# Optimization experiments

Measured on AMD Instinct MI355X. Metric: run time of the kernel, lower is better.

## Reference

```python
import jax, jax.numpy as jnp
import numpy as np

B, S, N, D, H = 4, 1024, 1024, 1024, 16
HD = D // H
EPS = 1e-5


def _xavier(key, shape):
    fan_in, fan_out = shape[1], shape[0]
    a = (6.0 / (fan_in + fan_out)) ** 0.5
    return jax.random.uniform(key, shape, jnp.float32, -a, a)


def layer_norm(x, g, b):
    m = jnp.mean(x, axis=-1, keepdims=True)
    v = jnp.mean(jnp.square(x - m), axis=-1, keepdims=True)
    return (x - m) * jax.lax.rsqrt(v + EPS) * g + b


def setup_inputs() -> dict:
    key = jax.random.key(0)
    ks = jax.random.split(key, 8)
    return {
        "x_q": jax.random.normal(ks[0], (B, S, D), jnp.float32),
        "x_k": jax.random.normal(ks[1], (B, N, D), jnp.float32),
        "x_v": jax.random.normal(ks[2], (B, N, D), jnp.float32),
        "Wq": _xavier(ks[3], (D, D)),
        "Wk": _xavier(ks[4], (D, D)),
        "Wv": _xavier(ks[5], (D, D)),
        "Wp": _xavier(ks[6], (D, D)),
        "qn_g": jnp.ones((HD,), jnp.float32),
        "qn_b": jnp.zeros((HD,), jnp.float32),
        "kn_g": jnp.ones((HD,), jnp.float32),
        "kn_b": jnp.zeros((HD,), jnp.float32),
        "on_g": jnp.ones((D,), jnp.float32),
        "on_b": jnp.zeros((D,), jnp.float32),
    }


def reference(x_q, x_k, x_v, Wq, Wk, Wv, Wp, qn_g, qn_b, kn_g, kn_b, on_g, on_b):
    scale = HD ** (-0.5)
    q = jnp.einsum('bsd,ed->bse', x_q, Wq)  # torch Linear: x @ W.T
    k = jnp.einsum('bnd,ed->bne', x_k, Wk)
    v = jnp.einsum('bnd,ed->bne', x_v, Wv)
    # Faithful to original: q is reshaped WITHOUT transpose (B,H,S,HD)
    q = q.reshape(B, H, S, HD)
    k = k.reshape(B, N, H, HD).transpose(0, 2, 1, 3)  # (B,H,N,HD)
    v = v.reshape(B, N, H, HD).transpose(0, 2, 1, 3)  # (B,H,N,HD)
    q = layer_norm(q, qn_g, qn_b) * scale
    k = layer_norm(k, kn_g, kn_b)
    attn = jax.nn.softmax(jnp.einsum('bhsd,bhnd->bhsn', q, k), axis=-1)
    x = jnp.einsum('bhsn,bhnd->bhsd', attn, v)
    x = x.transpose(0, 2, 1, 3).reshape(B, S, D)
    x = layer_norm(x, on_g, on_b)
    return jnp.einsum('bsd,ed->bse', x, Wp)
```

## Files before the change

### kernel.cpp

```cpp
#include <hip/hip_runtime.h>
#include <cstdint>

typedef unsigned short u16;
typedef __attribute__((ext_vector_type(4))) float f32x4;
typedef __attribute__((ext_vector_type(8))) short bf16x8;

__device__ __forceinline__ u16 f2bf(float f) {
  uint32_t u = __builtin_bit_cast(uint32_t, f);
  u += 0x7FFFu + ((u >> 16) & 1u);
  return (u16)(u >> 16);
}

__device__ __forceinline__ void gld16(const void* g, void* l) {
  __builtin_amdgcn_global_load_lds((const __attribute__((address_space(1))) void*)g,
                                   (__attribute__((address_space(3))) void*)l,
                                   16, 0, 0);
}

__global__ __launch_bounds__(256) void cast_all(const float* __restrict__ xq, const float* __restrict__ xk,
                                                const float* __restrict__ xv, const float* __restrict__ Wq,
                                                const float* __restrict__ Wk, const float* __restrict__ Wv,
                                                const float* __restrict__ Wp,
                                                u16* __restrict__ oq, u16* __restrict__ ok, u16* __restrict__ ov,
                                                u16* __restrict__ owq, u16* __restrict__ owk,
                                                u16* __restrict__ owv, u16* __restrict__ owp) {
  int bid = blockIdx.x;
  const float* src; u16* dst; size_t i;
  if (bid < 12288) {
    const int p = bid >> 12, ib = bid & 4095;
    src = (p == 0) ? xq : ((p == 1) ? xk : xv);
    dst = (p == 0) ? oq : ((p == 1) ? ok : ov);
    i = (size_t)ib * 256 + threadIdx.x;
  } else {
    bid -= 12288;
    const int p = bid >> 10, ib = bid & 1023;
    src = (p == 0) ? Wq : ((p == 1) ? Wk : ((p == 2) ? Wv : Wp));
    dst = (p == 0) ? owq : ((p == 1) ? owk : ((p == 2) ? owv : owp));
    i = (size_t)ib * 256 + threadIdx.x;
  }
  float4 v = *(const float4*)(src + i * 4);
  uint2 pk;
  pk.x = (uint32_t)f2bf(v.x) | ((uint32_t)f2bf(v.y) << 16);
  pk.y = (uint32_t)f2bf(v.z) | ((uint32_t)f2bf(v.w) << 16);
  *(uint2*)(dst + i * 4) = pk;
}

__device__ __forceinline__ void gemm_mainloop(const u16* __restrict__ A, const u16* __restrict__ B,
                                              int bm, int bn, u16* Al, u16* Bl,
                                              f32x4 (&acc)[2][4]) {
  const int t = threadIdx.x;
  const int w = t >> 6;
  const int lane = t & 63;
  const int l15 = lane & 15, l4 = lane >> 4;

  const u16* Ab = A + (size_t)bm * 128 * 1024;
  const u16* Bb = B + (size_t)bn * 64 * 1024;

  for (int kt = 0; kt < 1024; kt += 64) {
#pragma unroll
    for (int p = 0; p < 4; ++p) {
      const int idx = p * 256 + t;
      const int row = idx >> 3, ch = idx & 7;
      const int sch = ch ^ (row & 7);
      gld16(Ab + (size_t)row * 1024 + kt + sch * 8, (char*)Al + p * 4096 + (w << 10));
    }
#pragma unroll
    for (int p = 0; p < 2; ++p) {
      const int idx = p * 256 + t;
      const int row = idx >> 3, ch = idx & 7;
      const int sch = ch ^ (row & 7);
      gld16(Bb + (size_t)row * 1024 + kt + sch * 8, (char*)Bl + p * 4096 + (w << 10));
    }
    __syncthreads();
#pragma unroll
    for (int ks = 0; ks < 2; ++ks) {
      bf16x8 af[2], bfr[4];
#pragma unroll
      for (int mi = 0; mi < 2; ++mi) {
        const int row = w * 32 + mi * 16 + l15;
        const int ch = (ks * 4 + l4) ^ (row & 7);
        af[mi] = *(const bf16x8*)&Al[row * 64 + ch * 8];
      }
#pragma unroll
      for (int nj = 0; nj < 4; ++nj) {
        const int row = nj * 16 + l15;
        const int ch = (ks * 4 + l4) ^ (row & 7);
        bfr[nj] = *(const bf16x8*)&Bl[row * 64 + ch * 8];
      }
#pragma unroll
      for (int mi = 0; mi < 2; ++mi)
#pragma unroll
        for (int nj = 0; nj < 4; ++nj)
          acc[mi][nj] = __builtin_amdgcn_mfma_f32_16x16x32_bf16(af[mi], bfr[nj], acc[mi][nj], 0, 0, 0);
    }
    __syncthreads();
  }
}

__global__ __launch_bounds__(256) void gemm_qkv(const u16* __restrict__ A0, const u16* __restrict__ A1,
                                                const u16* __restrict__ A2, const u16* __restrict__ B0,
                                                const u16* __restrict__ B1, const u16* __restrict__ B2,
                                                u16* __restrict__ Qout, u16* __restrict__ Kout,
                                                u16* __restrict__ Vout,
                                                const float* __restrict__ qg, const float* __restrict__ qb,
                                                const float* __restrict__ kg, const float* __restrict__ kb) {
  __shared__ __align__(16) u16 Al[128 * 64];
  __shared__ __align__(16) u16 Bl[64 * 64];
  const int p = blockIdx.x >> 9;
  const int b0 = blockIdx.x & 511;
  const int bid = ((b0 & 7) << 6) + (b0 >> 3);
  const int bm = bid >> 4, bn = bid & 15;
  const u16* A = (p == 0) ? A0 : ((p == 1) ? A1 : A2);
  const u16* B = (p == 0) ? B0 : ((p == 1) ? B1 : B2);

  f32x4 acc[2][4];
#pragma unroll
  for (int i = 0; i < 2; ++i)
#pragma unroll
    for (int j = 0; j < 4; ++j) acc[i][j] = (f32x4){0.f, 0.f, 0.f, 0.f};

  gemm_mainloop(A, B, bm, bn, Al, Bl, acc);

  const int t = threadIdx.x, w = t >> 6, lane = t & 63;
  const int l15 = lane & 15, l4 = lane >> 4;
  const int c = bn;

  if (p == 2) {
#pragma unroll
    for (int mi = 0; mi < 2; ++mi) {
      const int n0 = bm * 128 + w * 32 + mi * 16 + l4 * 4;
      const int bi = n0 >> 10, ni = n0 & 1023;
      const int nt = ni >> 6, ng = (ni >> 3) & 7, no = ni & 7;
#pragma unroll
      for (int nj = 0; nj < 4; ++nj) {
        const int hd = nj * 16 + l15;
        uint32_t w0 = (uint32_t)f2bf(acc[mi][nj][0]) | ((uint32_t)f2bf(acc[mi][nj][1]) << 16);
        uint32_t w1 = (uint32_t)f2bf(acc[mi][nj][2]) | ((uint32_t)f2bf(acc[mi][nj][3]) << 16);
        uint2 pk = {w0, w1};
        const size_t addr = ((size_t)(bi * 16 + c) * 64 + hd) * 1024 + nt * 64 + ((ng ^ (hd & 7)) << 3) + no;
        *(uint2*)(Vout + addr) = pk;
      }
    }
    return;
  }

  const float scale = (p == 0) ? 0.18033688011112042f : 1.0f;
  const float* gv = (p == 0) ? qg : kg;
  const float* bv = (p == 0) ? qb : kb;
  u16* out = (p == 0) ? Qout : Kout;
  float gl[4], blc[4];
#pragma unroll
  for (int nj = 0; nj < 4; ++nj) {
    gl[nj] = gv[nj * 16 + l15];
    blc[nj] = bv[nj * 16 + l15] * scale;
  }
#pragma unroll
  for (int mi = 0; mi < 2; ++mi) {
#pragma unroll
    for (int r = 0; r < 4; ++r) {
      float s1 = 0.f, s2 = 0.f;
#pragma unroll
      for (int nj = 0; nj < 4; ++nj) {
        const float x = acc[mi][nj][r];
        s1 += x; s2 += x * x;
      }
#pragma unroll
      for (int mk = 1; mk < 16; mk <<= 1) {
        s1 += __shfl_xor(s1, mk, 64);
        s2 += __shfl_xor(s2, mk, 64);
      }
      const float mean = s1 * (1.0f / 64.0f);
      const float var = s2 * (1.0f / 64.0f) - mean * mean;
      const float rr = rsqrtf(var + 1e-5f) * scale;
      const int row_g = bm * 128 + w * 32 + mi * 16 + l4 * 4 + r;
      const int bi = row_g >> 10, rsi = row_g & 1023;
      size_t base; int sw;
      if (p == 0) {
        const int h = rsi >> 6;
        const int s2i = ((rsi & 63) << 4) + c;
        base = ((size_t)(bi * 16 + h) * 1024 + s2i) * 64;
        sw = (s2i & 7) << 3;
      } else {
        base = ((size_t)(bi * 16 + c) * 1024 + rsi) * 64;
        sw = (rsi & 7) << 3;
      }
#pragma unroll
      for (int nj = 0; nj < 4; ++nj) {
        const float y = (acc[mi][nj][r] - mean) * rr * gl[nj] + blc[nj];
        out[base + ((nj * 16 + l15) ^ sw)] = f2bf(y);
      }
    }
  }
}

__global__ __launch_bounds__(256) void gemm_p(const u16* __restrict__ A, const u16* __restrict__ B,
                                              float* __restrict__ C) {
  __shared__ __align__(16) u16 Al[128 * 64];
  __shared__ __align__(16) u16 Bl[64 * 64];
  const int bid = ((blockIdx.x & 7) << 6) + (blockIdx.x >> 3);
  const int bm = bid >> 4, bn = bid & 15;

  f32x4 acc[2][4];
#pragma unroll
  for (int i = 0; i < 2; ++i)
#pragma unroll
    for (int j = 0; j < 4; ++j) acc[i][j] = (f32x4){0.f, 0.f, 0.f, 0.f};

  gemm_mainloop(A, B, bm, bn, Al, Bl, acc);

  const int t = threadIdx.x, w = t >> 6, lane = t & 63;
  const int l15 = lane & 15, l4 = lane >> 4;
  float* Cb = C + (size_t)bm * 128 * 1024 + bn * 64;
#pragma unroll
  for (int mi = 0; mi < 2; ++mi)
#pragma unroll
    for (int nj = 0; nj < 4; ++nj) {
      const int row = w * 32 + mi * 16 + l4 * 4;
      const int col = nj * 16 + l15;
#pragma unroll
      for (int r = 0; r < 4; ++r)
        Cb[(size_t)(row + r) * 1024 + col] = acc[mi][nj][r];
    }
}

__global__ __launch_bounds__(256) void flash(const u16* __restrict__ Q,
                                             const u16* __restrict__ Km,
                                             const u16* __restrict__ Vt,
                                             float* __restrict__ ctx) {
  __shared__ __align__(16) u16 Kl[2 * 64 * 64];
  __shared__ __align__(16) u16 Vl[2 * 64 * 64];
  __shared__ __align__(16) u16 Pl[64 * 64];
  const int bid = ((blockIdx.x & 7) << 7) + (blockIdx.x >> 3);
  const int bh = bid >> 4, qt = bid & 15;
  const int t = threadIdx.x, w = t >> 6, lane = t & 63;
  const int l15 = lane & 15, l4 = lane >> 4;
  const int sx = (l15 & 7) << 3;
  const int ea0 = (l4 * 8) ^ sx;
  const int ea1 = ea0 ^ 32;

  const u16* Qrow = Q + ((size_t)bh * 1024 + qt * 64 + w * 16 + l15) * 64;
  const bf16x8 aq0 = *(const bf16x8*)(Qrow + ea0);
  const bf16x8 aq1 = *(const bf16x8*)(Qrow + ea1);
  const bf16x8 vone = {0x3F80, 0x3F80, 0x3F80, 0x3F80, 0x3F80, 0x3F80, 0x3F80, 0x3F80};

  const u16* Kg = Km + (size_t)bh * 65536;
  const u16* Vg = Vt + (size_t)bh * 65536;

  gld16((const char*)Kg + t * 16, (char*)Kl + (w << 10));
  gld16((const char*)Kg + 4096 + t * 16, (char*)Kl + 4096 + (w << 10));
  gld16(Vg + (t >> 3) * 1024 + (t & 7) * 8, (char*)Vl + (w << 10));
  gld16(Vg + ((t + 256) >> 3) * 1024 + (t & 7) * 8, (char*)Vl + 4096 + (w << 10));
  __syncthreads();

  f32x4 o[4];
  for (int i = 0; i < 4; ++i) o[i] = (f32x4){0.f, 0.f, 0.f, 0.f};
  f32x4 o4 = (f32x4){0.f, 0.f, 0.f, 0.f};

  int cur = 0;
  for (int nt2 = 0; nt2 < 16; ++nt2) {
    if (nt2 < 15) {
      const int nb = (cur ^ 1) * 8192;
      const char* ksrc = (const char*)(Kg + (size_t)(nt2 + 1) * 4096);
      gld16(ksrc + t * 16, (char*)Kl + nb + (w << 10));
      gld16(ksrc + 4096 + t * 16, (char*)Kl + nb + 4096 + (w << 10));
      gld16(Vg + (t >> 3) * 1024 + (nt2 + 1) * 64 + (t & 7) * 8, (char*)Vl + nb + (w << 10));
      gld16(Vg + ((t + 256) >> 3) * 1024 + (nt2 + 1) * 64 + (t & 7) * 8, (char*)Vl + nb + 4096 + (w << 10));
    }
    const u16* Kc = Kl + cur * 4096;
    const u16* Vc = Vl + cur * 4096;

    f32x4 sc[4];
    for (int cj = 0; cj < 4; ++cj) sc[cj] = (f32x4){0.f, 0.f, 0.f, 0.f};
#pragma unroll
    for (int ks = 0; ks < 2; ++ks) {
      const int ea = ks ? ea1 : ea0;
      const bf16x8 aq = ks ? aq1 : aq0;
#pragma unroll
      for (int cj = 0; cj < 4; ++cj) {
        bf16x8 bk = *(const bf16x8*)&Kc[(cj * 16 + l15) * 64 + ea];
        sc[cj] = __builtin_amdgcn_mfma_f32_16x16x32_bf16(aq, bk, sc[cj], 0, 0, 0);
      }
    }

#pragma unroll
    for (int cj = 0; cj < 4; ++cj)
#pragma unroll
      for (int r = 0; r < 4; ++r) {
        const float pf = __builtin_amdgcn_exp2f(sc[cj][r]);
        const uint32_t u = __builtin_bit_cast(uint32_t, pf);
        const int prow = w * 16 + l4 * 4 + r;
        Pl[prow * 64 + ((cj * 16 + l15) ^ (((l4 * 4 + r) & 7) << 3))] = (u16)((u + 0x8000u) >> 16);
      }

#pragma unroll
    for (int ks = 0; ks < 2; ++ks) {
      const int ea = ks ? ea1 : ea0;
      bf16x8 ap = *(const bf16x8*)&Pl[(w * 16 + l15) * 64 + ea];
#pragma unroll
      for (int c2 = 0; c2 < 4; ++c2) {
        bf16x8 bv = *(const bf16x8*)&Vc[(c2 * 16 + l15) * 64 + ea];
        o[c2] = __builtin_amdgcn_mfma_f32_16x16x32_bf16(ap, bv, o[c2], 0, 0, 0);
      }
      o4 = __builtin_amdgcn_mfma_f32_16x16x32_bf16(ap, vone, o4, 0, 0, 0);
    }
    __syncthreads();
    cur ^= 1;
  }

  const int b = bh >> 4, h = bh & 15;
#pragma unroll
  for (int c2 = 0; c2 < 4; ++c2) {
#pragma unroll
    for (int r = 0; r < 4; ++r) {
      const int s2 = qt * 64 + w * 16 + l4 * 4 + r;
      const int hd = c2 * 16 + l15;
      ctx[((size_t)b * 1024 + s2) * 1024 + h * 64 + hd] = o[c2][r] / o4[r];
    }
  }
}

__global__ __launch_bounds__(256) void ln_row(const float* __restrict__ X,
                                              const float* __restrict__ g,
                                              const float* __restrict__ bb,
                                              u16* __restrict__ out) {
  __shared__ float red[8];
  const int row = blockIdx.x, t = threadIdx.x;
  const int w = t >> 6, lane = t & 63;
  const float* xr = X + (size_t)row * 1024;
  float4 v = *(const float4*)(xr + t * 4);
  float s = v.x + v.y + v.z + v.w;
  for (int mk = 1; mk < 64; mk <<= 1) s += __shfl_xor(s, mk, 64);
  if (lane == 0) red[w] = s;
  __syncthreads();
  const float mean = (red[0] + red[1] + red[2] + red[3]) * (1.0f / 1024.0f);
  const float dx = v.x - mean, dy = v.y - mean, dz = v.z - mean, dw = v.w - mean;
  float q = dx * dx + dy * dy + dz * dz + dw * dw;
  for (int mk = 1; mk < 64; mk <<= 1) q += __shfl_xor(q, mk, 64);
  if (lane == 0) red[4 + w] = q;
  __syncthreads();
  const float var = (red[4] + red[5] + red[6] + red[7]) * (1.0f / 1024.0f);
  const float rs = rsqrtf(var + 1e-5f);
  float4 gg = *(const float4*)(g + t * 4);
  float4 b4 = *(const float4*)(bb + t * 4);
  uint2 pk;
  pk.x = (uint32_t)f2bf(dx * rs * gg.x + b4.x) | ((uint32_t)f2bf(dy * rs * gg.y + b4.y) << 16);
  pk.y = (uint32_t)f2bf(dz * rs * gg.z + b4.z) | ((uint32_t)f2bf(dw * rs * gg.w + b4.w) << 16);
  *(uint2*)(out + (size_t)row * 1024 + t * 4) = pk;
}

extern "C" void kernel_launch(void* const* d_in, const int* in_sizes, int n_in,
                              void* d_out, int out_size, void* d_ws, size_t ws_size,
                              hipStream_t stream) {
  (void)in_sizes; (void)n_in; (void)out_size; (void)ws_size;
  const float* x_q = (const float*)d_in[0];
  const float* x_k = (const float*)d_in[1];
  const float* x_v = (const float*)d_in[2];
  const float* Wq  = (const float*)d_in[3];
  const float* Wk  = (const float*)d_in[4];
  const float* Wv  = (const float*)d_in[5];
  const float* Wp  = (const float*)d_in[6];
  const float* qn_g = (const float*)d_in[7];
  const float* qn_b = (const float*)d_in[8];
  const float* kn_g = (const float*)d_in[9];
  const float* kn_b = (const float*)d_in[10];
  const float* on_g = (const float*)d_in[11];
  const float* on_b = (const float*)d_in[12];

  char* ws = (char*)d_ws;
  u16* xq_bf = (u16*)(ws + (0ull << 20));
  u16* xk_bf = (u16*)(ws + (8ull << 20));
  u16* xv_bf = (u16*)(ws + (16ull << 20));
  u16* Wq_bf = (u16*)(ws + (24ull << 20));
  u16* Wk_bf = (u16*)(ws + (26ull << 20));
  u16* Wv_bf = (u16*)(ws + (28ull << 20));
  u16* Wp_bf = (u16*)(ws + (30ull << 20));
  u16* Qa   = (u16*)(ws + (32ull << 20));
  u16* Ka   = (u16*)(ws + (40ull << 20));
  u16* Vtb  = (u16*)(ws + (48ull << 20));
  float* ctxf = (float*)(ws + (56ull << 20));
  u16* ctxb = (u16*)(ws + (72ull << 20));

  cast_all<<<16384, 256, 0, stream>>>(x_q, x_k, x_v, Wq, Wk, Wv, Wp,
                                      xq_bf, xk_bf, xv_bf, Wq_bf, Wk_bf, Wv_bf, Wp_bf);

  gemm_qkv<<<1536, 256, 0, stream>>>(xq_bf, xk_bf, xv_bf, Wq_bf, Wk_bf, Wv_bf,
                                     Qa, Ka, Vtb, qn_g, qn_b, kn_g, kn_b);
  flash<<<1024, 256, 0, stream>>>(Qa, Ka, Vtb, ctxf);
  ln_row<<<4096, 256, 0, stream>>>(ctxf, on_g, on_b, ctxb);
  gemm_p<<<512, 256, 0, stream>>>(ctxb, Wp_bf, (float*)d_out);
}
```

Measured before the change: 114.7 us.

## Load V directly from global into registers and store attention context as bf16

The V tile is no longer staged through shared memory. It is now written unswizzled by the QKV GEMM and each lane reads its bf16x8 fragments straight from global memory into registers every key tile. The flash kernel also writes its context output as bf16 instead of fp32, so the row layernorm reads half as many bytes. The aim is to cut LDS traffic and footprint and to halve the intermediate context bandwidth. The cost is uncoalesced, row-strided global loads of V that are not prefetched ahead of use, plus extra rounding of the context before layernorm.

Result: slower. 156.2 us (+36.1%).

```diff
diff --git a/kernel.cpp b/kernel.cpp
--- a/kernel.cpp
+++ b/kernel.cpp
@@ -130,15 +130,13 @@
     for (int mi = 0; mi < 2; ++mi) {
       const int n0 = bm * 128 + w * 32 + mi * 16 + l4 * 4;
       const int bi = n0 >> 10, ni = n0 & 1023;
-      const int nt = ni >> 6, ng = (ni >> 3) & 7, no = ni & 7;
 #pragma unroll
       for (int nj = 0; nj < 4; ++nj) {
         const int hd = nj * 16 + l15;
         uint32_t w0 = (uint32_t)f2bf(acc[mi][nj][0]) | ((uint32_t)f2bf(acc[mi][nj][1]) << 16);
         uint32_t w1 = (uint32_t)f2bf(acc[mi][nj][2]) | ((uint32_t)f2bf(acc[mi][nj][3]) << 16);
         uint2 pk = {w0, w1};
-        const size_t addr = ((size_t)(bi * 16 + c) * 64 + hd) * 1024 + nt * 64 + ((ng ^ (hd & 7)) << 3) + no;
-        *(uint2*)(Vout + addr) = pk;
+        *(uint2*)(Vout + ((size_t)(bi * 16 + c) * 64 + hd) * 1024 + ni) = pk;
       }
     }
     return;
@@ -226,9 +224,8 @@
 __global__ __launch_bounds__(256) void flash(const u16* __restrict__ Q,
                                              const u16* __restrict__ Km,
                                              const u16* __restrict__ Vt,
-                                             float* __restrict__ ctx) {
+                                             u16* __restrict__ ctxb) {
   __shared__ __align__(16) u16 Kl[2 * 64 * 64];
-  __shared__ __align__(16) u16 Vl[2 * 64 * 64];
   __shared__ __align__(16) u16 Pl[64 * 64];
   const int bid = ((blockIdx.x & 7) << 7) + (blockIdx.x >> 3);
   const int bh = bid >> 4, qt = bid & 15;
@@ -245,11 +242,10 @@
 
   const u16* Kg = Km + (size_t)bh * 65536;
   const u16* Vg = Vt + (size_t)bh * 65536;
+  const u16* Vrow = Vg + (size_t)l15 * 1024 + l4 * 8;
 
   gld16((const char*)Kg + t * 16, (char*)Kl + (w << 10));
   gld16((const char*)Kg + 4096 + t * 16, (char*)Kl + 4096 + (w << 10));
-  gld16(Vg + (t >> 3) * 1024 + (t & 7) * 8, (char*)Vl + (w << 10));
-  gld16(Vg + ((t + 256) >> 3) * 1024 + (t & 7) * 8, (char*)Vl + 4096 + (w << 10));
   __syncthreads();
 
   f32x4 o[4];
@@ -263,11 +259,15 @@
       const char* ksrc = (const char*)(Kg + (size_t)(nt2 + 1) * 4096);
       gld16(ksrc + t * 16, (char*)Kl + nb + (w << 10));
       gld16(ksrc + 4096 + t * 16, (char*)Kl + nb + 4096 + (w << 10));
-      gld16(Vg + (t >> 3) * 1024 + (nt2 + 1) * 64 + (t & 7) * 8, (char*)Vl + nb + (w << 10));
-      gld16(Vg + ((t + 256) >> 3) * 1024 + (nt2 + 1) * 64 + (t & 7) * 8, (char*)Vl + nb + 4096 + (w << 10));
-    }
+    }
+    bf16x8 bv[2][4];
+#pragma unroll
+    for (int ks = 0; ks < 2; ++ks)
+#pragma unroll
+      for (int c2 = 0; c2 < 4; ++c2)
+        bv[ks][c2] = *(const bf16x8*)(Vrow + (size_t)c2 * 16384 + nt2 * 64 + ks * 32);
+
     const u16* Kc = Kl + cur * 4096;
-    const u16* Vc = Vl + cur * 4096;
 
     f32x4 sc[4];
     for (int cj = 0; cj < 4; ++cj) sc[cj] = (f32x4){0.f, 0.f, 0.f, 0.f};
@@ -297,10 +297,8 @@
       const int ea = ks ? ea1 : ea0;
       bf16x8 ap = *(const bf16x8*)&Pl[(w * 16 + l15) * 64 + ea];
 #pragma unroll
-      for (int c2 = 0; c2 < 4; ++c2) {
-        bf16x8 bv = *(const bf16x8*)&Vc[(c2 * 16 + l15) * 64 + ea];
-        o[c2] = __builtin_amdgcn_mfma_f32_16x16x32_bf16(ap, bv, o[c2], 0, 0, 0);
-      }
+      for (int c2 = 0; c2 < 4; ++c2)
+        o[c2] = __builtin_amdgcn_mfma_f32_16x16x32_bf16(ap, bv[ks][c2], o[c2], 0, 0, 0);
       o4 = __builtin_amdgcn_mfma_f32_16x16x32_bf16(ap, vone, o4, 0, 0, 0);
     }
     __syncthreads();
@@ -314,26 +312,30 @@
     for (int r = 0; r < 4; ++r) {
       const int s2 = qt * 64 + w * 16 + l4 * 4 + r;
       const int hd = c2 * 16 + l15;
-      ctx[((size_t)b * 1024 + s2) * 1024 + h * 64 + hd] = o[c2][r] / o4[r];
-    }
-  }
-}
-
-__global__ __launch_bounds__(256) void ln_row(const float* __restrict__ X,
+      ctxb[((size_t)b * 1024 + s2) * 1024 + h * 64 + hd] = f2bf(o[c2][r] / o4[r]);
+    }
+  }
+}
+
+__global__ __launch_bounds__(256) void ln_row(const u16* __restrict__ X,
                                               const float* __restrict__ g,
                                               const float* __restrict__ bb,
                                               u16* __restrict__ out) {
   __shared__ float red[8];
   const int row = blockIdx.x, t = threadIdx.x;
   const int w = t >> 6, lane = t & 63;
-  const float* xr = X + (size_t)row * 1024;
-  float4 v = *(const float4*)(xr + t * 4);
-  float s = v.x + v.y + v.z + v.w;
+  const u16* xr = X + (size_t)row * 1024;
+  ushort4 uv = *(const ushort4*)(xr + t * 4);
+  float x0 = __builtin_bit_cast(float, (uint32_t)uv.x << 16);
+  float x1 = __builtin_bit_cast(float, (uint32_t)uv.y << 16);
+  float x2 = __builtin_bit_cast(float, (uint32_t)uv.z << 16);
+  float x3 = __builtin_bit_cast(float, (uint32_t)uv.w << 16);
+  float s = x0 + x1 + x2 + x3;
   for (int mk = 1; mk < 64; mk <<= 1) s += __shfl_xor(s, mk, 64);
   if (lane == 0) red[w] = s;
   __syncthreads();
   const float mean = (red[0] + red[1] + red[2] + red[3]) * (1.0f / 1024.0f);
-  const float dx = v.x - mean, dy = v.y - mean, dz = v.z - mean, dw = v.w - mean;
+  const float dx = x0 - mean, dy = x1 - mean, dz = x2 - mean, dw = x3 - mean;
   float q = dx * dx + dy * dy + dz * dz + dw * dw;
   for (int mk = 1; mk < 64; mk <<= 1) q += __shfl_xor(q, mk, 64);
   if (lane == 0) red[4 + w] = q;
@@ -377,15 +379,15 @@
   u16* Qa   = (u16*)(ws + (32ull << 20));
   u16* Ka   = (u16*)(ws + (40ull << 20));
   u16* Vtb  = (u16*)(ws + (48ull << 20));
-  float* ctxf = (float*)(ws + (56ull << 20));
-  u16* ctxb = (u16*)(ws + (72ull << 20));
+  u16* ctxb = (u16*)(ws + (56ull << 20));
+  u16* ctx2 = (u16*)(ws + (64ull << 20));
 
   cast_all<<<16384, 256, 0, stream>>>(x_q, x_k, x_v, Wq, Wk, Wv, Wp,
                                       xq_bf, xk_bf, xv_bf, Wq_bf, Wk_bf, Wv_bf, Wp_bf);
 
   gemm_qkv<<<1536, 256, 0, stream>>>(xq_bf, xk_bf, xv_bf, Wq_bf, Wk_bf, Wv_bf,
                                      Qa, Ka, Vtb, qn_g, qn_b, kn_g, kn_b);
-  flash<<<1024, 256, 0, stream>>>(Qa, Ka, Vtb, ctxf);
-  ln_row<<<4096, 256, 0, stream>>>(ctxf, on_g, on_b, ctxb);
-  gemm_p<<<512, 256, 0, stream>>>(ctxb, Wp_bf, (float*)d_out);
-}
+  flash<<<1024, 256, 0, stream>>>(Qa, Ka, Vtb, ctxb);
+  ln_row<<<4096, 256, 0, stream>>>(ctxb, on_g, on_b, ctx2);
+  gemm_p<<<512, 256, 0, stream>>>(ctx2, Wp_bf, (float*)d_out);
+}
```
